# Kernel optimization log

Measured on AMD Instinct MI355X. Metric: run time of the kernel, lower is better.

Reference implementation:

```python
import jax, jax.numpy as jnp
import numpy as np

N_NODES = 50000
N_EDGES = 800000
NUM_FEATS = 512
NUM_CLASSES = 64
NUM_LAYERS = 4


def setup_inputs() -> dict:
    key = jax.random.key(0)
    k1, k2, k3 = jax.random.split(key, 3)
    x = jax.random.normal(k1, (N_NODES, NUM_FEATS), dtype=jnp.float32)
    # glorot init for weight [num_feats, num_classes]
    scale = jnp.sqrt(6.0 / (NUM_FEATS + NUM_CLASSES)).astype(jnp.float32)
    weight = jax.random.uniform(k2, (NUM_FEATS, NUM_CLASSES), dtype=jnp.float32,
                                minval=-scale, maxval=scale)
    edge_index = jax.random.randint(k3, (2, N_EDGES), 0, N_NODES, dtype=jnp.int64)
    return {"x": x, "weight": weight, "edge_index": edge_index}


def reference(x, weight, edge_index):
    row, col = edge_index[0], edge_index[1]  # [E], [E]
    # symmetric GCN normalization: deg^{-1/2}[row] * deg^{-1/2}[col]
    deg = jax.ops.segment_sum(jnp.ones((edge_index.shape[1],), dtype=x.dtype),
                              row, num_segments=x.shape[0])  # [N]
    deg_inv_sqrt = jnp.where(deg > 0, jax.lax.rsqrt(jnp.maximum(deg, 1e-12)), 0.0)
    norm = (deg_inv_sqrt[row] * deg_inv_sqrt[col])[:, None]  # [E, 1]

    h = x @ weight  # [N, num_classes] (dropout skipped: eval mode)
    for _ in range(NUM_LAYERS):
        # gather source features, scale by edge norm, scatter-add to destinations
        msg = norm * h[row]  # [E, num_classes]
        h = jax.ops.segment_sum(msg, col, num_segments=x.shape[0])  # [N, num_classes]
        # type_norm == 'None' -> layers_bn is identity
    return h
```

## Files before the change

### kernel.cpp

```cpp
#include <hip/hip_runtime.h>
#include <hip/hip_fp16.h>

#define NFEAT 512
#define NCLS  64
#define NNODES 50000
#define NW    (NNODES / 4)
#define NB    256
#define NG    8
#define SLOTS 64

typedef unsigned int uint;
typedef unsigned short ushort;
using short8 = __attribute__((ext_vector_type(8))) short;
using f32x4  = __attribute__((ext_vector_type(4))) float;

static __device__ __forceinline__ unsigned short f32_to_bf16_rne(float f) {
    unsigned u = __float_as_uint(f);
    unsigned r = u + 0x7FFFu + ((u >> 16) & 1u);
    return (unsigned short)(r >> 16);
}
static __device__ __forceinline__ float bf16_to_f32(unsigned short b) {
    return __uint_as_float(((unsigned)b) << 16);
}
static __device__ __forceinline__ uint cvt_pk_bf16(float a, float b) {
    uint r;
    asm("v_cvt_pk_bf16_f32 %0, %1, %2" : "=v"(r) : "v"(a), "v"(b));
    return r;
}
static __device__ __forceinline__ void split_bf16x8(const float* xs, short8& ahi, short8& alo) {
    union { uint u[4]; short8 s; } H, L;
#pragma unroll
    for (int t = 0; t < 4; ++t) {
        float x0 = xs[2 * t], x1 = xs[2 * t + 1];
        uint hp = cvt_pk_bf16(x0, x1);
        float f0 = __uint_as_float(hp << 16);
        float f1 = __uint_as_float(hp & 0xffff0000u);
        uint lp = cvt_pk_bf16(x0 - f0, x1 - f1);
        H.u[t] = hp; L.u[t] = lp;
    }
    ahi = H.s; alo = L.s;
}


__global__ __launch_bounds__(256) void hist_packw_kernel(
        const int* __restrict__ row, const int* __restrict__ col,
        const float* __restrict__ w,
        uint* __restrict__ degB, uint* __restrict__ cntB,
        short8* __restrict__ wp, int E, int CH) {
    __shared__ __align__(16) uint h[2 * NW];
    int b = blockIdx.x;
    if (b < NB) {
        for (int i = threadIdx.x; i < 2 * NW; i += 256) h[i] = 0;
        __syncthreads();
        int e0 = b * CH, e1 = min(E, e0 + CH);
        for (int e = e0 + threadIdx.x; e < e1; e += 256) {
            int c = col[e], r = row[e];
            atomicAdd(&h[c >> 2], 1u << ((c & 3) * 8));
            atomicAdd(&h[NW + (r >> 2)], 1u << ((r & 3) * 8));
        }
        __syncthreads();
        uint4* cb = reinterpret_cast<uint4*>(cntB + (size_t)b * NW);
        uint4* db = reinterpret_cast<uint4*>(degB + (size_t)b * NW);
        const uint4* c4 = reinterpret_cast<const uint4*>(h);
        const uint4* d4 = reinterpret_cast<const uint4*>(h + NW);
        for (int i = threadIdx.x; i < NW / 4; i += 256) cb[i] = c4[i];
        for (int i = threadIdx.x; i < NW / 4; i += 256) db[i] = d4[i];
        return;
    }
    int gid = (b - NB) * 256 + threadIdx.x;
    int lane = gid & 63;
    int F = gid >> 6;
    int s = F & 1;
    int nt = (F >> 1) & 3;
    int kk = F >> 3;
    int k0 = kk * 32 + (lane >> 4) * 8;
    int c  = nt * 16 + (lane & 15);
    short8 v;
#pragma unroll
    for (int j = 0; j < 8; ++j) {
        float xv = w[(k0 + j) * NCLS + c];
        unsigned short hi = f32_to_bf16_rne(xv);
        unsigned short outv = hi;
        if (s) outv = f32_to_bf16_rne(xv - bf16_to_f32(hi));
        v[j] = (short)outv;
    }
    wp[gid] = v;
}


__global__ __launch_bounds__(256) void scan_sub_kernel(uint* __restrict__ cntB,
                                                       const uint* __restrict__ degB,
                                                       uint* __restrict__ cntSub,
                                                       uint* __restrict__ degSub) {
    int gid = blockIdx.x * 256 + threadIdx.x;
    if (gid >= 2 * NG * NW) return;
    int half = gid / (NG * NW);
    int rem  = gid % (NG * NW);
    int g = rem / NW, wi = rem % NW;
    if (half == 0) {
        uint run = 0;
#pragma unroll 8
        for (int b = g * 32; b < g * 32 + 32; ++b) {
            uint v = cntB[(size_t)b * NW + wi];
            cntB[(size_t)b * NW + wi] = run;
            run += v;
        }
        cntSub[(size_t)g * NW + wi] = run;
    } else {
        uint run = 0;
#pragma unroll 8
        for (int b = g * 32; b < g * 32 + 32; ++b) run += degB[(size_t)b * NW + wi];
        degSub[(size_t)g * NW + wi] = run;
    }
}


__global__ __launch_bounds__(256) void scan_top_kernel(uint* __restrict__ cntSub,
                                                       const uint* __restrict__ degSub,
                                                       int* __restrict__ cntTot,
                                                       float* __restrict__ dinv) {
    int wi = blockIdx.x * 256 + threadIdx.x;
    if (wi >= NW) return;
    uint run = 0;
#pragma unroll
    for (int g = 0; g < NG; ++g) {
        uint v = cntSub[(size_t)g * NW + wi];
        cntSub[(size_t)g * NW + wi] = run;
        run += v;
    }
    int4 t = { (int)(run & 255), (int)((run >> 8) & 255),
               (int)((run >> 16) & 255), (int)(run >> 24) };
    *reinterpret_cast<int4*>(cntTot + wi * 4) = t;

    uint run2 = 0;
#pragma unroll
    for (int g = 0; g < NG; ++g) run2 += degSub[(size_t)g * NW + wi];
    int d0 = run2 & 255, d1 = (run2 >> 8) & 255, d2 = (run2 >> 16) & 255, d3 = run2 >> 24;
    float4 dv;
    dv.x = d0 ? rsqrtf((float)d0) : 0.0f;
    dv.y = d1 ? rsqrtf((float)d1) : 0.0f;
    dv.z = d2 ? rsqrtf((float)d2) : 0.0f;
    dv.w = d3 ? rsqrtf((float)d3) : 0.0f;
    *reinterpret_cast<float4*>(dinv + wi * 4) = dv;
}


__global__ __launch_bounds__(256, 2) void place_matmul_kernel(
        const int* __restrict__ row, const int* __restrict__ col,
        const uint* __restrict__ offB, const uint* __restrict__ cntSub,
        ushort* __restrict__ slots,
        const float* __restrict__ x, const short8* __restrict__ wp,
        const float* __restrict__ dinv, __half* __restrict__ u0,
        int N, int E, int CH) {
    __shared__ __align__(16) uint sh[NW];
    int b = blockIdx.x;

    if (b < NB) {
        uint4* c4 = reinterpret_cast<uint4*>(sh);
        const uint4* o4 = reinterpret_cast<const uint4*>(offB + (size_t)b * NW);
        const uint4* s4 = reinterpret_cast<const uint4*>(cntSub + (size_t)(b >> 5) * NW);
        for (int i = threadIdx.x; i < NW / 4; i += 256) {
            uint4 a = o4[i], d = s4[i];
            a.x += d.x; a.y += d.y; a.z += d.z; a.w += d.w;
            c4[i] = a;
        }
        __syncthreads();
        int e0 = b * CH, e1 = min(E, e0 + CH);
        for (int e = e0 + threadIdx.x; e < e1; e += 256) {
            int c = col[e];
            uint old = atomicAdd(&sh[c >> 2], 1u << ((c & 3) * 8));
            int pos = (old >> ((c & 3) * 8)) & 255;
            if (pos < SLOTS)
                __builtin_nontemporal_store((ushort)row[e], &slots[(c << 6) + pos]);
        }
        return;
    }

    int tile = b - NB;
    int tid = threadIdx.x;
    int wave = tid >> 6, lane = tid & 63;
    int rlo = lane & 15, khi = lane >> 4;
    int row0 = tile * 128 + wave * 32;

    size_t roff[2];
#pragma unroll
    for (int rg = 0; rg < 2; ++rg) {
        int rr = row0 + rg * 16 + rlo;
        if (rr > N - 1) rr = N - 1;
        roff[rg] = (size_t)rr * NFEAT + khi * 8;
    }

    f32x4 acc[2][4];
#pragma unroll
    for (int rg = 0; rg < 2; ++rg)
#pragma unroll
        for (int nt = 0; nt < 4; ++nt) acc[rg][nt] = f32x4{0.f, 0.f, 0.f, 0.f};

    const short8* fbase = wp + lane;
    for (int ch = 0; ch < 4; ++ch) {
#pragma unroll
        for (int kk = 0; kk < 4; ++kk) {
            const short8* fb = fbase + ch * 2048 + kk * 512;
            short8 bh0 = fb[0],   bl0 = fb[64];
            short8 bh1 = fb[128], bl1 = fb[192];
            short8 bh2 = fb[256], bl2 = fb[320];
            short8 bh3 = fb[384], bl3 = fb[448];
            int kg = ch * 128 + kk * 32;
#pragma unroll
            for (int rg = 0; rg < 2; ++rg) {
                float4 xa = *reinterpret_cast<const float4*>(x + roff[rg] + kg);
                float4 xb = *reinterpret_cast<const float4*>(x + roff[rg] + kg + 4);
                float xs[8] = {xa.x, xa.y, xa.z, xa.w, xb.x, xb.y, xb.z, xb.w};
                short8 ahi, alo;
                split_bf16x8(xs, ahi, alo);
                acc[rg][0] = __builtin_amdgcn_mfma_f32_16x16x32_bf16(ahi, bh0, acc[rg][0], 0, 0, 0);
                acc[rg][1] = __builtin_amdgcn_mfma_f32_16x16x32_bf16(ahi, bh1, acc[rg][1], 0, 0, 0);
                acc[rg][2] = __builtin_amdgcn_mfma_f32_16x16x32_bf16(ahi, bh2, acc[rg][2], 0, 0, 0);
                acc[rg][3] = __builtin_amdgcn_mfma_f32_16x16x32_bf16(ahi, bh3, acc[rg][3], 0, 0, 0);
                acc[rg][0] = __builtin_amdgcn_mfma_f32_16x16x32_bf16(alo, bh0, acc[rg][0], 0, 0, 0);
                acc[rg][1] = __builtin_amdgcn_mfma_f32_16x16x32_bf16(alo, bh1, acc[rg][1], 0, 0, 0);
                acc[rg][2] = __builtin_amdgcn_mfma_f32_16x16x32_bf16(alo, bh2, acc[rg][2], 0, 0, 0);
                acc[rg][3] = __builtin_amdgcn_mfma_f32_16x16x32_bf16(alo, bh3, acc[rg][3], 0, 0, 0);
                acc[rg][0] = __builtin_amdgcn_mfma_f32_16x16x32_bf16(ahi, bl0, acc[rg][0], 0, 0, 0);
                acc[rg][1] = __builtin_amdgcn_mfma_f32_16x16x32_bf16(ahi, bl1, acc[rg][1], 0, 0, 0);
                acc[rg][2] = __builtin_amdgcn_mfma_f32_16x16x32_bf16(ahi, bl2, acc[rg][2], 0, 0, 0);
                acc[rg][3] = __builtin_amdgcn_mfma_f32_16x16x32_bf16(ahi, bl3, acc[rg][3], 0, 0, 0);
            }
        }
    }

#pragma unroll
    for (int rg = 0; rg < 2; ++rg) {
        int rbase = row0 + rg * 16 + khi * 4;
#pragma unroll
        for (int j = 0; j < 4; ++j) {
            int r = rbase + j;
            if (r < N) {
                float dn = dinv[r];
                __half* op = u0 + ((size_t)r << 6) + rlo;
                op[0]  = __float2half(acc[rg][0][j] * dn);
                op[16] = __float2half(acc[rg][1][j] * dn);
                op[32] = __float2half(acc[rg][2][j] * dn);
                op[48] = __float2half(acc[rg][3][j] * dn);
            }
        }
    }
}


__global__ __launch_bounds__(256) void gather_kernel(const __half* __restrict__ u,
                                                     const int* __restrict__ cntTot,
                                                     ushort* __restrict__ slots,
                                                     const float* __restrict__ dinv,
                                                     __half* __restrict__ out_h,
                                                     float* __restrict__ out_f,
                                                     int N, int sq, int dosort) {
    int wave = threadIdx.x >> 6, lane = threadIdx.x & 63;
    int q = lane >> 3;
    int p = lane & 7;
    int wbase = blockIdx.x * 8 + wave * 2;
    if (wbase >= N) return;

    int sv[2], cqv[2];
    float acc[2][8];
#pragma unroll
    for (int nn = 0; nn < 2; ++nn) {
        int wid = wbase + nn;
        sv[nn] = 0xFFFF; cqv[nn] = 0;
        if (wid < N) {
            int cq = cntTot[wid];
            cqv[nn] = (cq < SLOTS) ? cq : SLOTS;
            sv[nn] = slots[((size_t)wid << 6) + lane];
        }
#pragma unroll
        for (int t = 0; t < 8; ++t) acc[nn][t] = 0.f;
    }

    if (dosort) {
#pragma unroll
        for (int nn = 0; nn < 2; ++nn) {
            int wid = wbase + nn;
            if (wid >= N) continue;
            int v = (lane < cqv[nn]) ? sv[nn] : 0xFFFF;
#pragma unroll
            for (int k = 2; k <= 64; k <<= 1) {
#pragma unroll
                for (int j = k >> 1; j >= 1; j >>= 1) {
                    int pv = __shfl_xor(v, j);
                    int lo = min(v, pv), hi = max(v, pv);
                    bool up = ((lane & k) == 0);
                    v = (((lane & j) == 0) == up) ? lo : hi;
                }
            }
            sv[nn] = v;
            if (lane < cqv[nn]) slots[((size_t)wid << 6) + lane] = (ushort)v;
        }
    }

#pragma unroll
    for (int j = 0; j < 8; ++j) {
        int idx = q + 8 * j;
#pragma unroll
        for (int nn = 0; nn < 2; ++nn) {
            int s = __shfl(sv[nn], idx);
            if (idx < cqv[nn]) {
                uint4 d = *reinterpret_cast<const uint4*>(u + ((size_t)s << 6) + p * 8);
                float2 f0 = __half22float2(*reinterpret_cast<__half2*>(&d.x));
                float2 f1 = __half22float2(*reinterpret_cast<__half2*>(&d.y));
                float2 f2 = __half22float2(*reinterpret_cast<__half2*>(&d.z));
                float2 f3 = __half22float2(*reinterpret_cast<__half2*>(&d.w));
                acc[nn][0] += f0.x; acc[nn][1] += f0.y;
                acc[nn][2] += f1.x; acc[nn][3] += f1.y;
                acc[nn][4] += f2.x; acc[nn][5] += f2.y;
                acc[nn][6] += f3.x; acc[nn][7] += f3.y;
            }
        }
    }

#pragma unroll
    for (int off = 8; off < 64; off <<= 1) {
#pragma unroll
        for (int nn = 0; nn < 2; ++nn)
#pragma unroll
            for (int t = 0; t < 8; ++t)
                acc[nn][t] += __shfl_xor(acc[nn][t], off);
    }

    if (q == 0) {
#pragma unroll
        for (int nn = 0; nn < 2; ++nn) {
            int wid = wbase + nn;
            if (wid >= N) continue;
            float sc = dinv[wid];
            if (sq) {
                float s2 = sc * sc;
                __half2 h0 = __floats2half2_rn(acc[nn][0] * s2, acc[nn][1] * s2);
                __half2 h1 = __floats2half2_rn(acc[nn][2] * s2, acc[nn][3] * s2);
                __half2 h2 = __floats2half2_rn(acc[nn][4] * s2, acc[nn][5] * s2);
                __half2 h3 = __floats2half2_rn(acc[nn][6] * s2, acc[nn][7] * s2);
                uint4 d;
                d.x = *reinterpret_cast<uint*>(&h0);
                d.y = *reinterpret_cast<uint*>(&h1);
                d.z = *reinterpret_cast<uint*>(&h2);
                d.w = *reinterpret_cast<uint*>(&h3);
                *reinterpret_cast<uint4*>(out_h + ((size_t)wid << 6) + p * 8) = d;
            } else {
                float4 r0 = {acc[nn][0] * sc, acc[nn][1] * sc, acc[nn][2] * sc, acc[nn][3] * sc};
                float4 r1 = {acc[nn][4] * sc, acc[nn][5] * sc, acc[nn][6] * sc, acc[nn][7] * sc};
                float4* op = reinterpret_cast<float4*>(out_f + ((size_t)wid << 6) + p * 8);
                op[0] = r0;
                op[1] = r1;
            }
        }
    }
}


extern "C" void kernel_launch(void* const* d_in, const int* in_sizes, int n_in,
                              void* d_out, int out_size, void* d_ws, size_t ws_size,
                              hipStream_t stream) {
    const float* x = (const float*)d_in[0];
    const float* w = (const float*)d_in[1];
    const int*   ei = (const int*)d_in[2];

    int N = in_sizes[0] / NFEAT;
    int E = in_sizes[2] / 2;
    const int* row = ei;
    const int* col = ei + E;
    float* out = (float*)d_out;

    auto align256 = [](size_t v) { return (v + 255) & ~(size_t)255; };
    char* ws = (char*)d_ws;
    size_t off = 0;
    uint* cntB   = (uint*)(ws + off);   off += align256((size_t)NB * NW * sizeof(uint));
    uint* degB   = (uint*)(ws + off);   off += align256((size_t)NB * NW * sizeof(uint));
    uint* cntSub = (uint*)(ws + off);   off += align256((size_t)NG * NW * sizeof(uint));
    uint* degSub = (uint*)(ws + off);   off += align256((size_t)NG * NW * sizeof(uint));
    int* cntTot  = (int*)(ws + off);    off += align256((size_t)NNODES * sizeof(int));
    float* dinv  = (float*)(ws + off);  off += align256((size_t)NNODES * sizeof(float));
    short8* wp   = (short8*)(ws + off); off += align256((size_t)8192 * sizeof(short8));
    ushort* slots = (ushort*)(ws + off); off += align256((size_t)NNODES * SLOTS * sizeof(ushort));
    __half* uA   = (__half*)(ws + off); off += align256((size_t)NNODES * NCLS * sizeof(__half));
    __half* uB   = (__half*)(ws + off); off += align256((size_t)NNODES * NCLS * sizeof(__half));

    int CH = (E + NB - 1) / NB;

    hist_packw_kernel<<<NB + 32, 256, 0, stream>>>(row, col, w, degB, cntB, wp, E, CH);
    scan_sub_kernel<<<(2 * NG * NW + 255) / 256, 256, 0, stream>>>(cntB, degB, cntSub, degSub);
    scan_top_kernel<<<(NW + 255) / 256, 256, 0, stream>>>(cntSub, degSub, cntTot, dinv);
    int nmm = (N + 127) / 128;
    place_matmul_kernel<<<NB + nmm, 256, 0, stream>>>(row, col, cntB, cntSub, slots,
                                                      x, wp, dinv, uA, N, E, CH);

    int ngrid = (N + 7) / 8;
    gather_kernel<<<ngrid, 256, 0, stream>>>(uA, cntTot, slots, dinv, uB, nullptr, N, 1, 1);
    gather_kernel<<<ngrid, 256, 0, stream>>>(uB, cntTot, slots, dinv, uA, nullptr, N, 1, 0);
    gather_kernel<<<ngrid, 256, 0, stream>>>(uA, cntTot, slots, dinv, uB, nullptr, N, 1, 0);
    gather_kernel<<<ngrid, 256, 0, stream>>>(uB, cntTot, slots, dinv, nullptr, out, N, 0, 0);
}
```

Measured before the change: 166.4 us.

## Replace per-block column count histograms with two-level binned CSR construction

Drops the 256 per-block column-count histograms and their prefix scan, and instead bins edges into 196 coarse destination bins of 256 nodes each. Each bin then builds its node slot lists in shared memory and writes them out with wide coalesced stores. The aim is to cut the large workspace traffic of the histograms and the scattered 2-byte global slot stores. In exchange it adds a memset, a block-local sort through LDS, and a fixed per-bin capacity, so edges beyond that cap are silently dropped if a bin overflows.

```diff
diff --git a/kernel.cpp b/kernel.cpp
--- a/kernel.cpp
+++ b/kernel.cpp
@@ -8,6 +8,10 @@
 #define NB    256
 #define NG    8
 #define SLOTS 64
+#define BINS  196
+#define BCAP  4864
+#define NODEPAD (BINS * 256)
+#define CH    3125
 
 typedef unsigned int uint;
 typedef unsigned short ushort;
@@ -42,32 +46,63 @@
 }
 
 
-__global__ __launch_bounds__(256) void hist_packw_kernel(
+__global__ __launch_bounds__(256, 2) void bin_packw_kernel(
         const int* __restrict__ row, const int* __restrict__ col,
         const float* __restrict__ w,
-        uint* __restrict__ degB, uint* __restrict__ cntB,
-        short8* __restrict__ wp, int E, int CH) {
-    __shared__ __align__(16) uint h[2 * NW];
+        uint* __restrict__ degB, uint* __restrict__ binCur, uint* __restrict__ binBuf,
+        short8* __restrict__ wp, int E) {
+    __shared__ __align__(16) uint degh[NW];
+    __shared__ uint sortedE[CH + 3];
+    __shared__ uint hist[BINS], bstart[BINS], baseg[BINS], lcur[BINS];
+    __shared__ uint tmp[256];
     int b = blockIdx.x;
+    int tid = threadIdx.x;
+
     if (b < NB) {
-        for (int i = threadIdx.x; i < 2 * NW; i += 256) h[i] = 0;
+        for (int i = tid; i < NW; i += 256) degh[i] = 0;
+        if (tid < BINS) { hist[tid] = 0; lcur[tid] = 0; }
         __syncthreads();
         int e0 = b * CH, e1 = min(E, e0 + CH);
-        for (int e = e0 + threadIdx.x; e < e1; e += 256) {
+        for (int e = e0 + tid; e < e1; e += 256) {
             int c = col[e], r = row[e];
-            atomicAdd(&h[c >> 2], 1u << ((c & 3) * 8));
-            atomicAdd(&h[NW + (r >> 2)], 1u << ((r & 3) * 8));
-        }
-        __syncthreads();
-        uint4* cb = reinterpret_cast<uint4*>(cntB + (size_t)b * NW);
+            atomicAdd(&hist[c >> 8], 1u);
+            atomicAdd(&degh[r >> 2], 1u << ((r & 3) * 8));
+        }
+        __syncthreads();
+        uint v = (tid < BINS) ? hist[tid] : 0;
+        uint xs = v;
+        tmp[tid] = xs; __syncthreads();
+        for (int d = 1; d < 256; d <<= 1) {
+            uint u = (tid >= d) ? tmp[tid - d] : 0;
+            __syncthreads();
+            xs += u; tmp[tid] = xs;
+            __syncthreads();
+        }
+        if (tid < BINS) {
+            bstart[tid] = xs - v;
+            baseg[tid] = atomicAdd(&binCur[tid], v);
+        }
+        __syncthreads();
+        for (int e = e0 + tid; e < e1; e += 256) {
+            int c = col[e], r = row[e];
+            int bin = c >> 8;
+            uint idx = bstart[bin] + atomicAdd(&lcur[bin], 1u);
+            sortedE[idx] = ((uint)bin << 24) | ((uint)(c & 255) << 16) | (uint)r;
+        }
+        __syncthreads();
+        int cnt = e1 - e0;
+        for (int i = tid; i < cnt; i += 256) {
+            uint en = sortedE[i];
+            int bin = en >> 24;
+            uint gpos = baseg[bin] + (uint)i - bstart[bin];
+            if (gpos < BCAP) binBuf[(size_t)bin * BCAP + gpos] = en & 0xFFFFFFu;
+        }
         uint4* db = reinterpret_cast<uint4*>(degB + (size_t)b * NW);
-        const uint4* c4 = reinterpret_cast<const uint4*>(h);
-        const uint4* d4 = reinterpret_cast<const uint4*>(h + NW);
-        for (int i = threadIdx.x; i < NW / 4; i += 256) cb[i] = c4[i];
-        for (int i = threadIdx.x; i < NW / 4; i += 256) db[i] = d4[i];
+        const uint4* d4 = reinterpret_cast<const uint4*>(degh);
+        for (int i = tid; i < NW / 4; i += 256) db[i] = d4[i];
         return;
     }
-    int gid = (b - NB) * 256 + threadIdx.x;
+    int gid = (b - NB) * 256 + tid;
     int lane = gid & 63;
     int F = gid >> 6;
     int s = F & 1;
@@ -88,54 +123,25 @@
 }
 
 
-__global__ __launch_bounds__(256) void scan_sub_kernel(uint* __restrict__ cntB,
-                                                       const uint* __restrict__ degB,
-                                                       uint* __restrict__ cntSub,
-                                                       uint* __restrict__ degSub) {
+__global__ __launch_bounds__(256) void deg_sub_kernel(const uint* __restrict__ degB,
+                                                      uint* __restrict__ degSub) {
     int gid = blockIdx.x * 256 + threadIdx.x;
-    if (gid >= 2 * NG * NW) return;
-    int half = gid / (NG * NW);
-    int rem  = gid % (NG * NW);
-    int g = rem / NW, wi = rem % NW;
-    if (half == 0) {
-        uint run = 0;
+    if (gid >= NG * NW) return;
+    int g = gid / NW, wi = gid % NW;
+    uint run = 0;
 #pragma unroll 8
-        for (int b = g * 32; b < g * 32 + 32; ++b) {
-            uint v = cntB[(size_t)b * NW + wi];
-            cntB[(size_t)b * NW + wi] = run;
-            run += v;
-        }
-        cntSub[(size_t)g * NW + wi] = run;
-    } else {
-        uint run = 0;
-#pragma unroll 8
-        for (int b = g * 32; b < g * 32 + 32; ++b) run += degB[(size_t)b * NW + wi];
-        degSub[(size_t)g * NW + wi] = run;
-    }
-}
-
-
-__global__ __launch_bounds__(256) void scan_top_kernel(uint* __restrict__ cntSub,
-                                                       const uint* __restrict__ degSub,
-                                                       int* __restrict__ cntTot,
-                                                       float* __restrict__ dinv) {
+    for (int b = g * 32; b < g * 32 + 32; ++b) run += degB[(size_t)b * NW + wi];
+    degSub[(size_t)g * NW + wi] = run;
+}
+
+__global__ __launch_bounds__(256) void deg_top_kernel(const uint* __restrict__ degSub,
+                                                      float* __restrict__ dinv) {
     int wi = blockIdx.x * 256 + threadIdx.x;
     if (wi >= NW) return;
     uint run = 0;
 #pragma unroll
-    for (int g = 0; g < NG; ++g) {
-        uint v = cntSub[(size_t)g * NW + wi];
-        cntSub[(size_t)g * NW + wi] = run;
-        run += v;
-    }
-    int4 t = { (int)(run & 255), (int)((run >> 8) & 255),
-               (int)((run >> 16) & 255), (int)(run >> 24) };
-    *reinterpret_cast<int4*>(cntTot + wi * 4) = t;
-
-    uint run2 = 0;
-#pragma unroll
-    for (int g = 0; g < NG; ++g) run2 += degSub[(size_t)g * NW + wi];
-    int d0 = run2 & 255, d1 = (run2 >> 8) & 255, d2 = (run2 >> 16) & 255, d3 = run2 >> 24;
+    for (int g = 0; g < NG; ++g) run += degSub[(size_t)g * NW + wi];
+    int d0 = run & 255, d1 = (run >> 8) & 255, d2 = (run >> 16) & 255, d3 = run >> 24;
     float4 dv;
     dv.x = d0 ? rsqrtf((float)d0) : 0.0f;
     dv.y = d1 ? rsqrtf((float)d1) : 0.0f;
@@ -145,39 +151,40 @@
 }
 
 
-__global__ __launch_bounds__(256, 2) void place_matmul_kernel(
-        const int* __restrict__ row, const int* __restrict__ col,
-        const uint* __restrict__ offB, const uint* __restrict__ cntSub,
-        ushort* __restrict__ slots,
+__global__ __launch_bounds__(256, 4) void bin_matmul_kernel(
+        const uint* __restrict__ binCur, const uint* __restrict__ binBuf,
+        ushort* __restrict__ slots, int* __restrict__ cntTot,
         const float* __restrict__ x, const short8* __restrict__ wp,
-        const float* __restrict__ dinv, __half* __restrict__ u0,
-        int N, int E, int CH) {
-    __shared__ __align__(16) uint sh[NW];
+        const float* __restrict__ dinv, __half* __restrict__ u0, int N) {
+    __shared__ __align__(16) ushort lslots[256 * SLOTS];
+    __shared__ uint lcnt[256];
     int b = blockIdx.x;
-
-    if (b < NB) {
-        uint4* c4 = reinterpret_cast<uint4*>(sh);
-        const uint4* o4 = reinterpret_cast<const uint4*>(offB + (size_t)b * NW);
-        const uint4* s4 = reinterpret_cast<const uint4*>(cntSub + (size_t)(b >> 5) * NW);
-        for (int i = threadIdx.x; i < NW / 4; i += 256) {
-            uint4 a = o4[i], d = s4[i];
-            a.x += d.x; a.y += d.y; a.z += d.z; a.w += d.w;
-            c4[i] = a;
-        }
-        __syncthreads();
-        int e0 = b * CH, e1 = min(E, e0 + CH);
-        for (int e = e0 + threadIdx.x; e < e1; e += 256) {
-            int c = col[e];
-            uint old = atomicAdd(&sh[c >> 2], 1u << ((c & 3) * 8));
-            int pos = (old >> ((c & 3) * 8)) & 255;
-            if (pos < SLOTS)
-                __builtin_nontemporal_store((ushort)row[e], &slots[(c << 6) + pos]);
-        }
+    int tid = threadIdx.x;
+
+    if (b < BINS) {
+        lcnt[tid] = 0;
+        __syncthreads();
+        int total = (int)binCur[b];
+        if (total > BCAP) total = BCAP;
+        const uint* bb = binBuf + (size_t)b * BCAP;
+        for (int i = tid; i < total; i += 256) {
+            uint en = bb[i];
+            int cl = (en >> 16) & 255;
+            uint pos = atomicAdd(&lcnt[cl], 1u);
+            if (pos < SLOTS) lslots[(cl << 6) + pos] = (ushort)(en & 0xFFFFu);
+        }
+        __syncthreads();
+        int n0 = b << 8;
+        uint4* gs = reinterpret_cast<uint4*>(slots + ((size_t)n0 << 6));
+        const uint4* ls = reinterpret_cast<const uint4*>(lslots);
+        for (int i = tid; i < 256 * SLOTS * 2 / 16; i += 256) gs[i] = ls[i];
+        int n = n0 + tid;
+        uint cv = lcnt[tid];
+        cntTot[n] = (cv < SLOTS) ? (int)cv : SLOTS;
         return;
     }
 
-    int tile = b - NB;
-    int tid = threadIdx.x;
+    int tile = b - BINS;
     int wave = tid >> 6, lane = tid & 63;
     int rlo = lane & 15, khi = lane >> 4;
     int row0 = tile * 128 + wave * 32;
@@ -210,9 +217,9 @@
             for (int rg = 0; rg < 2; ++rg) {
                 float4 xa = *reinterpret_cast<const float4*>(x + roff[rg] + kg);
                 float4 xb = *reinterpret_cast<const float4*>(x + roff[rg] + kg + 4);
-                float xs[8] = {xa.x, xa.y, xa.z, xa.w, xb.x, xb.y, xb.z, xb.w};
+                float xsv[8] = {xa.x, xa.y, xa.z, xa.w, xb.x, xb.y, xb.z, xb.w};
                 short8 ahi, alo;
-                split_bf16x8(xs, ahi, alo);
+                split_bf16x8(xsv, ahi, alo);
                 acc[rg][0] = __builtin_amdgcn_mfma_f32_16x16x32_bf16(ahi, bh0, acc[rg][0], 0, 0, 0);
                 acc[rg][1] = __builtin_amdgcn_mfma_f32_16x16x32_bf16(ahi, bh1, acc[rg][1], 0, 0, 0);
                 acc[rg][2] = __builtin_amdgcn_mfma_f32_16x16x32_bf16(ahi, bh2, acc[rg][2], 0, 0, 0);
@@ -372,25 +379,25 @@
     auto align256 = [](size_t v) { return (v + 255) & ~(size_t)255; };
     char* ws = (char*)d_ws;
     size_t off = 0;
-    uint* cntB   = (uint*)(ws + off);   off += align256((size_t)NB * NW * sizeof(uint));
-    uint* degB   = (uint*)(ws + off);   off += align256((size_t)NB * NW * sizeof(uint));
-    uint* cntSub = (uint*)(ws + off);   off += align256((size_t)NG * NW * sizeof(uint));
-    uint* degSub = (uint*)(ws + off);   off += align256((size_t)NG * NW * sizeof(uint));
-    int* cntTot  = (int*)(ws + off);    off += align256((size_t)NNODES * sizeof(int));
-    float* dinv  = (float*)(ws + off);  off += align256((size_t)NNODES * sizeof(float));
-    short8* wp   = (short8*)(ws + off); off += align256((size_t)8192 * sizeof(short8));
-    ushort* slots = (ushort*)(ws + off); off += align256((size_t)NNODES * SLOTS * sizeof(ushort));
-    __half* uA   = (__half*)(ws + off); off += align256((size_t)NNODES * NCLS * sizeof(__half));
-    __half* uB   = (__half*)(ws + off); off += align256((size_t)NNODES * NCLS * sizeof(__half));
-
-    int CH = (E + NB - 1) / NB;
-
-    hist_packw_kernel<<<NB + 32, 256, 0, stream>>>(row, col, w, degB, cntB, wp, E, CH);
-    scan_sub_kernel<<<(2 * NG * NW + 255) / 256, 256, 0, stream>>>(cntB, degB, cntSub, degSub);
-    scan_top_kernel<<<(NW + 255) / 256, 256, 0, stream>>>(cntSub, degSub, cntTot, dinv);
+    uint* degB    = (uint*)(ws + off);   off += align256((size_t)NB * NW * sizeof(uint));
+    uint* degSub  = (uint*)(ws + off);   off += align256((size_t)NG * NW * sizeof(uint));
+    float* dinv   = (float*)(ws + off);  off += align256((size_t)NNODES * sizeof(float));
+    int* cntTot   = (int*)(ws + off);    off += align256((size_t)NODEPAD * sizeof(int));
+    short8* wp    = (short8*)(ws + off); off += align256((size_t)8192 * sizeof(short8));
+    uint* binCur  = (uint*)(ws + off);   off += align256((size_t)BINS * sizeof(uint));
+    uint* binBuf  = (uint*)(ws + off);   off += align256((size_t)BINS * BCAP * sizeof(uint));
+    ushort* slots = (ushort*)(ws + off); off += align256((size_t)NODEPAD * SLOTS * sizeof(ushort));
+    __half* uA    = (__half*)(ws + off); off += align256((size_t)NNODES * NCLS * sizeof(__half));
+    __half* uB    = (__half*)(ws + off); off += align256((size_t)NNODES * NCLS * sizeof(__half));
+
+    hipMemsetAsync(binCur, 0, (size_t)BINS * sizeof(uint), stream);
+
+    bin_packw_kernel<<<NB + 32, 256, 0, stream>>>(row, col, w, degB, binCur, binBuf, wp, E);
+    deg_sub_kernel<<<(NG * NW + 255) / 256, 256, 0, stream>>>(degB, degSub);
+    deg_top_kernel<<<(NW + 255) / 256, 256, 0, stream>>>(degSub, dinv);
     int nmm = (N + 127) / 128;
-    place_matmul_kernel<<<NB + nmm, 256, 0, stream>>>(row, col, cntB, cntSub, slots,
-                                                      x, wp, dinv, uA, N, E, CH);
+    bin_matmul_kernel<<<BINS + nmm, 256, 0, stream>>>(binCur, binBuf, slots, cntTot,
+                                                      x, wp, dinv, uA, N);
 
     int ngrid = (N + 7) / 8;
     gather_kernel<<<ngrid, 256, 0, stream>>>(uA, cntTot, slots, dinv, uB, nullptr, N, 1, 1);
```

New measurement: 159.4 us. 1.04x faster.
